# Kernel tuning notes

Measured on AMD Instinct MI355X. Metric: run time of the kernel, lower is better.

The kernel has to match this reference:

```python
import jax, jax.numpy as jnp
import numpy as np

B, L, S, D, H = 2, 384, 384, 512, 256
BASE_TEMP = 10.0
LN_EPS = 1e-5


def setup_inputs() -> dict:
    key = jax.random.key(0)
    ks = jax.random.split(key, 12)
    return {
        "q": jax.random.normal(ks[0], (B, L, D), jnp.float32),
        "k": jax.random.normal(ks[1], (B, S, D), jnp.float32),
        "q_global": jax.random.normal(ks[2], (B, D), jnp.float32),
        "k_global": jax.random.normal(ks[3], (B, D), jnp.float32),
        "W1": jax.random.normal(ks[4], (4 * D, H), jnp.float32) * (1.0 / np.sqrt(4 * D)),
        "b1": jnp.zeros((H,), jnp.float32),
        "gamma": jnp.ones((H,), jnp.float32),
        "beta": jnp.zeros((H,), jnp.float32),
        "W2": jax.random.normal(ks[5], (H, 1), jnp.float32) * (1.0 / np.sqrt(H)),
        "b2": jnp.zeros((1,), jnp.float32),
        "gumbel_u": jax.random.uniform(ks[6], (B, L, S, 2), jnp.float32),
    }


def reference(q, k, q_global, k_global, W1, b1, gamma, beta, W2, b2, gumbel_u):
    d = q.shape[-1]
    # Decompose Linear(4D,H) on the [q, k, q_global, k_global] concat into
    # four per-tensor projections; sum broadcasts to the pairwise grid.
    Wq, Wk, Wqg, Wkg = jnp.split(W1, 4, axis=0)  # each [D,H]
    hq = q @ Wq + (q_global @ Wqg)[:, None, :]   # [B,L,H]
    hk = k @ Wk + (k_global @ Wkg)[:, None, :]   # [B,S,H]
    h = hq[:, :, None, :] + hk[:, None, :, :] + b1  # [B,L,S,H]
    h = jax.nn.gelu(h, approximate=False)
    mu = jnp.mean(h, axis=-1, keepdims=True)
    var = jnp.mean(jnp.square(h - mu), axis=-1, keepdims=True)
    h = (h - mu) * jax.lax.rsqrt(var + LN_EPS) * gamma + beta
    thresholds = (h @ W2)[..., 0] + b2[0]  # [B,L,S]
    sim = jnp.einsum("bld,bsd->bls", q, k) / jnp.sqrt(jnp.float32(d))
    logits = (sim - thresholds) / BASE_TEMP
    binary_logits = jnp.stack([-logits, logits], axis=-1)  # [B,L,S,2]
    u = jnp.clip(gumbel_u, 1e-6, 1.0 - 1e-6)
    g = -jnp.log(-jnp.log(u))
    soft = jax.nn.softmax(binary_logits + g, axis=-1)  # tau=1.0
    hard = jax.nn.one_hot(jnp.argmax(soft, axis=-1), 2, dtype=soft.dtype)
    y = hard + soft - jax.lax.stop_gradient(soft)  # straight-through
    return y[..., 1][:, None, :, :]  # [B,1,L,S]
```

## Files before the change

kernel.cpp:

```cpp
#include <hip/hip_runtime.h>
#include <hip/hip_bf16.h>
#include <math.h>

#define Bb 2
#define Lq 384
#define Sk 384
#define Dd 512
#define Hh 256

#define LIST_CAP 65536
#define NROWS (2 * Bb * Lq)

#define HQD_OFF  0
#define HKD_OFF  (HQD_OFF + Bb*Lq*Hh*8)
#define PART_OFF (HKD_OFF + Bb*Sk*Hh*8)
#define GQD_OFF  (PART_OFF + NROWS*4*Hh*8)
#define GKD_OFF  (GQD_OFF + Bb*Hh*8)
#define HQ_OFF   (GKD_OFF + Bb*Hh*8)
#define HK_OFF   (HQ_OFF + Bb*Lq*Hh*4)
#define SIM0_OFF (HK_OFF + Bb*Sk*Hh*4)
#define SIM1_OFF (SIM0_OFF + Bb*Lq*Sk*4)
#define SCAL_OFF (SIM1_OFF + Bb*Lq*Sk*4)
#define CNT_OFF  (SCAL_OFF + 64)
#define LIST_OFF (CNT_OFF + 64)

__global__ __launch_bounds__(256) void smalls_kernel(
    const float* __restrict__ qg, const float* __restrict__ kg,
    const float* __restrict__ W1,
    const float* __restrict__ gam, const float* __restrict__ bet,
    const float* __restrict__ W2, const float* __restrict__ b2,
    double* __restrict__ gq_d, double* __restrict__ gk_d,
    float* __restrict__ scal, int* __restrict__ cnt)
{
    __shared__ double red[64][5];
    __shared__ float2 red2[256];
    int bx  = blockIdx.x;
    int tid = threadIdx.x;
    if (bx < 16) {
        int isK = bx & 1;
        int b   = (bx >> 1) & 1;
        int hc  = bx >> 2;
        int hl  = tid >> 2;
        int dp  = tid & 3;
        int h   = hc * 64 + hl;
        const float* gv = (isK ? kg : qg) + b * Dd;
        const float* wp = W1 + (isK ? 3 : 2) * Dd * Hh + h;
        int d0 = dp * 128;
        double a0 = 0, a1 = 0, a2 = 0, a3 = 0;
        for (int i = 0; i < 128; i += 4) {
            int d = d0 + i;
            a0 = fma((double)gv[d + 0], (double)wp[(d + 0) * Hh], a0);
            a1 = fma((double)gv[d + 1], (double)wp[(d + 1) * Hh], a1);
            a2 = fma((double)gv[d + 2], (double)wp[(d + 2) * Hh], a2);
            a3 = fma((double)gv[d + 3], (double)wp[(d + 3) * Hh], a3);
        }
        red[hl][dp] = ((a0 + a1) + (a2 + a3));
        __syncthreads();
        if (dp == 0) {
            double s = (red[hl][0] + red[hl][1]) + (red[hl][2] + red[hl][3]);
            (isK ? gk_d : gq_d)[b * Hh + h] = s;
        }
    } else {
        if (tid == 0) *cnt = 0;
        float w2v = W2[tid];
        red2[tid] = make_float2(gam[tid] * w2v, bet[tid] * w2v);
        __syncthreads();
        for (int o = 128; o > 0; o >>= 1) {
            if (tid < o) {
                red2[tid].x += red2[tid + o].x;
                red2[tid].y += red2[tid + o].y;
            }
            __syncthreads();
        }
        if (tid == 0) {
            scal[0] = red2[0].x;
            scal[1] = red2[0].y + b2[0];
        }
    }
}

__global__ __launch_bounds__(256) void projd_part_kernel(
    const float* __restrict__ q, const float* __restrict__ k,
    const float* __restrict__ W1, double* __restrict__ part)
{
    __shared__ __align__(16) float tile[4][128];
    int tid = threadIdx.x;
    int bx  = blockIdx.x;
    int ds  = bx & 3;
    int rgid = bx >> 2;
    bool isQ = rgid < 192;
    int bb = isQ ? rgid : rgid - 192;
    int b  = bb / 96;
    int rg = bb % 96;
    const float* src = isQ ? q : k;
    int woff = isQ ? 0 : Dd * Hh;
    int rowbase = b * Lq + rg * 4;

    if (tid < 128) {
        int row = tid >> 5;
        int c4  = (tid & 31) << 2;
        *reinterpret_cast<float4*>(&tile[row][c4]) =
            *reinterpret_cast<const float4*>(
                src + (size_t)(rowbase + row) * Dd + ds * 128 + c4);
    }
    __syncthreads();

    const float* wp = W1 + woff + (ds * 128) * Hh + tid;
    double a0 = 0.0, a1 = 0.0, a2 = 0.0, a3 = 0.0;
#pragma unroll 2
    for (int d4 = 0; d4 < 128; d4 += 4) {
        double w0 = (double)wp[(d4 + 0) * Hh];
        double w1 = (double)wp[(d4 + 1) * Hh];
        double w2 = (double)wp[(d4 + 2) * Hh];
        double w3 = (double)wp[(d4 + 3) * Hh];
        float4 t0 = *reinterpret_cast<const float4*>(&tile[0][d4]);
        float4 t1 = *reinterpret_cast<const float4*>(&tile[1][d4]);
        float4 t2 = *reinterpret_cast<const float4*>(&tile[2][d4]);
        float4 t3 = *reinterpret_cast<const float4*>(&tile[3][d4]);
        a0 = fma((double)t0.x, w0, a0); a0 = fma((double)t0.y, w1, a0);
        a0 = fma((double)t0.z, w2, a0); a0 = fma((double)t0.w, w3, a0);
        a1 = fma((double)t1.x, w0, a1); a1 = fma((double)t1.y, w1, a1);
        a1 = fma((double)t1.z, w2, a1); a1 = fma((double)t1.w, w3, a1);
        a2 = fma((double)t2.x, w0, a2); a2 = fma((double)t2.y, w1, a2);
        a2 = fma((double)t2.z, w2, a2); a2 = fma((double)t2.w, w3, a2);
        a3 = fma((double)t3.x, w0, a3); a3 = fma((double)t3.y, w1, a3);
        a3 = fma((double)t3.z, w2, a3); a3 = fma((double)t3.w, w3, a3);
    }
    int rowglob = (isQ ? 0 : Bb * Lq) + rowbase;
    size_t obase = ((size_t)rowglob * 4 + ds) * Hh + tid;
    part[obase]            = a0;
    part[obase + 4 * Hh]   = a1;
    part[obase + 8 * Hh]   = a2;
    part[obase + 12 * Hh]  = a3;
}

__global__ __launch_bounds__(256) void finalize_kernel(
    const double* __restrict__ part,
    const double* __restrict__ gq_d, const double* __restrict__ gk_d,
    const float* __restrict__ b1,
    double* __restrict__ hq_d, double* __restrict__ hk_d,
    float* __restrict__ hq, float* __restrict__ hk)
{
    int tid = threadIdx.x;
    int bx  = blockIdx.x;
#pragma unroll
    for (int r = 0; r < 2; ++r) {
        int rowglob = bx * 2 + r;
        bool isQ = rowglob < Bb * Lq;
        int rr = isQ ? rowglob : rowglob - Bb * Lq;
        int b  = rr / Lq;
        size_t pbase = ((size_t)rowglob * 4) * Hh + tid;
        double p0 = part[pbase];
        double p1 = part[pbase + 1 * Hh];
        double p2 = part[pbase + 2 * Hh];
        double p3 = part[pbase + 3 * Hh];
        double gl = (isQ ? gq_d : gk_d)[b * Hh + tid];
        double tot = ((p0 + p1) + (p2 + p3)) + gl;
        size_t o = (size_t)rr * Hh + tid;
        if (isQ) {
            hq_d[o] = tot;
            hq[o]   = (float)(tot + (double)b1[tid]);
        } else {
            hk_d[o] = tot;
            hk[o]   = (float)tot;
        }
    }
}

__global__ __launch_bounds__(256) void sim_kernel(
    const float* __restrict__ q, const float* __restrict__ k,
    float* __restrict__ sim01)
{
    __shared__ __align__(16) float qs[32][132];
    __shared__ __align__(16) float ks[32][132];
    int tid = threadIdx.x;
    int bx = blockIdx.x;
    int kc = (bx >= Bb * 144) ? 1 : 0;
    int r  = bx - kc * Bb * 144;
    int b  = r / 144;  r %= 144;
    int lt = r / 12, st = r % 12;
    int tl = tid >> 4, ts = tid & 15;
    const float* qb = q + (b * Lq + lt * 32) * Dd;
    const float* kb = k + (b * Sk + st * 32) * Dd;
    float a00 = 0.f, a01 = 0.f, a10 = 0.f, a11 = 0.f;
    for (int c = kc * 256; c < kc * 256 + 256; c += 128) {
        __syncthreads();
        for (int i = tid; i < 1024; i += 256) {
            int row = i >> 5;
            int c4  = (i & 31) << 2;
            *reinterpret_cast<float4*>(&qs[row][c4]) =
                *reinterpret_cast<const float4*>(qb + row * Dd + c + c4);
            *reinterpret_cast<float4*>(&ks[row][c4]) =
                *reinterpret_cast<const float4*>(kb + row * Dd + c + c4);
        }
        __syncthreads();
#pragma unroll 2
        for (int dd = 0; dd < 128; dd += 4) {
            float4 q0 = *reinterpret_cast<const float4*>(&qs[tl][dd]);
            float4 q1 = *reinterpret_cast<const float4*>(&qs[tl + 16][dd]);
            float4 k0 = *reinterpret_cast<const float4*>(&ks[ts][dd]);
            float4 k1 = *reinterpret_cast<const float4*>(&ks[ts + 16][dd]);
            a00 = fmaf(q0.x, k0.x, a00); a00 = fmaf(q0.y, k0.y, a00);
            a00 = fmaf(q0.z, k0.z, a00); a00 = fmaf(q0.w, k0.w, a00);
            a01 = fmaf(q0.x, k1.x, a01); a01 = fmaf(q0.y, k1.y, a01);
            a01 = fmaf(q0.z, k1.z, a01); a01 = fmaf(q0.w, k1.w, a01);
            a10 = fmaf(q1.x, k0.x, a10); a10 = fmaf(q1.y, k0.y, a10);
            a10 = fmaf(q1.z, k0.z, a10); a10 = fmaf(q1.w, k0.w, a10);
            a11 = fmaf(q1.x, k1.x, a11); a11 = fmaf(q1.y, k1.y, a11);
            a11 = fmaf(q1.z, k1.z, a11); a11 = fmaf(q1.w, k1.w, a11);
        }
    }
    const float sc = 0.04419417382415922f;
    float* dst = sim01 + kc * (Bb * Lq * Sk);
    int l0 = lt * 32 + tl, s0 = st * 32 + ts;
    dst[(b * Lq + l0)      * Sk + s0]      = a00 * sc;
    dst[(b * Lq + l0)      * Sk + s0 + 16] = a01 * sc;
    dst[(b * Lq + l0 + 16) * Sk + s0]      = a10 * sc;
    dst[(b * Lq + l0 + 16) * Sk + s0 + 16] = a11 * sc;
}

__device__ __forceinline__ void gelu2(float2 hqv, float2 hkv, float2 gwv,
                                      float2& s1, float2& s2, float2& sw)
{
    const float P2   = 0.23164189f;
    const float A1f = 0.254829592f, A2f = -0.284496736f, A3f = 1.421413741f,
                A4f = -1.453152027f, A5f = 1.061405429f;
    const float NL2EH = -0.72134752044448170f;

    float xa = hqv.x + hkv.x,        xb = hqv.y + hkv.y;
    float axa = fabsf(xa),           axb = fabsf(xb);
    float dda = fmaf(P2, axa, 1.0f), ddb = fmaf(P2, axb, 1.0f);
    float ta = __builtin_amdgcn_rcpf(dda), tb = __builtin_amdgcn_rcpf(ddb);
    float x2a = xa * xa,             x2b = xb * xb;
    float exa = __builtin_amdgcn_exp2f(x2a * NL2EH);
    float exb = __builtin_amdgcn_exp2f(x2b * NL2EH);
    float sa = fmaf(A5f, ta, A4f),   sb = fmaf(A5f, tb, A4f);
    sa = fmaf(sa, ta, A3f);          sb = fmaf(sb, tb, A3f);
    sa = fmaf(sa, ta, A2f);          sb = fmaf(sb, tb, A2f);
    sa = fmaf(sa, ta, A1f);          sb = fmaf(sb, tb, A1f);
    sa = sa * ta;                    sb = sb * tb;
    float Ea = fmaf(-sa, exa, 1.0f), Eb = fmaf(-sb, exb, 1.0f);
    float ya = fmaf(axa, Ea, xa),    yb = fmaf(axb, Eb, xb);
    s1.x += ya;                      s1.y += yb;
    s2.x = fmaf(ya, ya, s2.x);       s2.y = fmaf(yb, yb, s2.y);
    sw.x = fmaf(ya, gwv.x, sw.x);    sw.y = fmaf(yb, gwv.y, sw.y);
}

__global__ __launch_bounds__(256) void main_kernel(
    const float* __restrict__ hq, const float* __restrict__ hk,
    const float* __restrict__ sim0, const float* __restrict__ sim1,
    const float* __restrict__ gam, const float* __restrict__ W2,
    const float* __restrict__ scal,
    const float* __restrict__ gu, float* __restrict__ out,
    int* __restrict__ cnt, int* __restrict__ list)
{
    __shared__ __align__(16) float hq_t[32][260];
    __shared__ __align__(16) float hk_t[16][260];
    __shared__ __align__(16) float gw_s[256];
    int tid = threadIdx.x;
    int bx = blockIdx.x;
    int b  = bx / (12 * 24);
    int r  = bx % (12 * 24);
    int lt = r / 24, st = r % 24;

    const float* hqb = hq + (b * Lq + lt * 32) * Hh;
    const float* hkb = hk + (b * Sk + st * 16) * Hh;
#pragma unroll
    for (int i = 0; i < 8; ++i) {
        int idx4 = i * 256 + tid;
        int row  = idx4 >> 6;
        int col4 = (idx4 & 63) << 2;
        *reinterpret_cast<float4*>(&hq_t[row][col4]) =
            *reinterpret_cast<const float4*>(hqb + row * Hh + col4);
    }
#pragma unroll
    for (int i = 0; i < 4; ++i) {
        int idx4 = i * 256 + tid;
        int row  = idx4 >> 6;
        int col4 = (idx4 & 63) << 2;
        *reinterpret_cast<float4*>(&hk_t[row][col4]) =
            *reinterpret_cast<const float4*>(hkb + row * Hh + col4);
    }
    gw_s[tid] = gam[tid] * W2[tid];
    __syncthreads();
    float gwsum  = scal[0];
    float bconst = scal[1];

    int tl = tid >> 4, ts = tid & 15;
    float2 s1a = make_float2(0.f, 0.f), s2a = s1a, swa = s1a;
    float2 s1b = s1a, s2b = s1a, swb = s1a;
#pragma unroll 2
    for (int h4 = 0; h4 < Hh; h4 += 4) {
        float4 ha = *reinterpret_cast<const float4*>(&hq_t[tl][h4]);
        float4 hb = *reinterpret_cast<const float4*>(&hq_t[tl + 16][h4]);
        float4 kk = *reinterpret_cast<const float4*>(&hk_t[ts][h4]);
        float4 g4 = *reinterpret_cast<const float4*>(&gw_s[h4]);
        gelu2(make_float2(ha.x, ha.y), make_float2(kk.x, kk.y),
              make_float2(g4.x, g4.y), s1a, s2a, swa);
        gelu2(make_float2(ha.z, ha.w), make_float2(kk.z, kk.w),
              make_float2(g4.z, g4.w), s1a, s2a, swa);
        gelu2(make_float2(hb.x, hb.y), make_float2(kk.x, kk.y),
              make_float2(g4.x, g4.y), s1b, s2b, swb);
        gelu2(make_float2(hb.z, hb.w), make_float2(kk.z, kk.w),
              make_float2(g4.z, g4.w), s1b, s2b, swb);
    }

#pragma unroll
    for (int e = 0; e < 2; ++e) {
        float S1 = e ? (s1b.x + s1b.y) : (s1a.x + s1a.y);
        float S2 = e ? (s2b.x + s2b.y) : (s2a.x + s2a.y);
        float SW = 0.5f * (e ? (swb.x + swb.y) : (swa.x + swa.y));
        float mu   = S1 * (1.0f / 512.0f);
        float var  = S2 * (1.0f / 1024.0f) - mu * mu;
        float rstd = rsqrtf(var + 1e-5f);
        float thr  = rstd * (SW - mu * gwsum) + bconst;

        int l = lt * 32 + tl + e * 16, s = st * 16 + ts;
        int idx = (b * Lq + l) * Sk + s;
        float  sv = sim0[idx] + sim1[idx];
        float2 uv = reinterpret_cast<const float2*>(gu)[idx];
        float u0 = fminf(fmaxf(uv.x, 1e-6f), 1.0f - 1e-6f);
        float u1 = fminf(fmaxf(uv.y, 1e-6f), 1.0f - 1e-6f);
        float g0 = -logf(-logf(u0));
        float g1 = -logf(-logf(u1));
        float t  = 0.2f * (sv - thr) + (g1 - g0);
        out[idx] = t > 0.0f ? 1.0f : 0.0f;
        if (fabsf(t) < 1e-3f) {
            int p = atomicAdd(cnt, 1);
            if (p < LIST_CAP) list[p] = idx;
        }
    }
}

__global__ __launch_bounds__(256) void cleanup_kernel(
    const float* __restrict__ q, const float* __restrict__ k,
    const double* __restrict__ hq_d, const double* __restrict__ hk_d,
    const float* __restrict__ b1,
    const float* __restrict__ gam, const float* __restrict__ bet,
    const float* __restrict__ W2, const float* __restrict__ b2,
    const float* __restrict__ gu, float* __restrict__ out,
    const int* __restrict__ cnt, const int* __restrict__ list)
{
    __shared__ double s0[256], s1[256], s2[256], s3[256];
    int tid = threadIdx.x;
    int n = *cnt;
    if (n > LIST_CAP) n = LIST_CAP;
    if (n == 0) return;

    double gw  = (double)gam[tid] * (double)W2[tid];
    double b1d = (double)b1[tid];
    s0[tid] = (double)bet[tid] * (double)W2[tid];
    s1[tid] = gw;
    __syncthreads();
    for (int o = 128; o > 0; o >>= 1) {
        if (tid < o) { s0[tid] += s0[tid + o]; s1[tid] += s1[tid + o]; }
        __syncthreads();
    }
    double bconst = s0[0] + (double)b2[0];
    double gwsum  = s1[0];
    __syncthreads();

    for (int it = blockIdx.x; it < n; it += gridDim.x) {
        int idx = list[it];
        int b   = idx / (Lq * Sk);
        int rem = idx % (Lq * Sk);
        int l = rem / Sk, s = rem % Sk;
        double x = (hq_d[(b * Lq + l) * Hh + tid]
                  + hk_d[(b * Sk + s) * Hh + tid]) + b1d;
        double y = 0.5 * x * (1.0 + erf(x * 0.70710678118654752440));
        const float* qrow = q + (b * Lq + l) * Dd;
        const float* krow = k + (b * Sk + s) * Dd;
        double sp = (double)qrow[tid] * (double)krow[tid]
                  + (double)qrow[tid + 256] * (double)krow[tid + 256];
        s0[tid] = y; s1[tid] = y * y; s2[tid] = y * gw; s3[tid] = sp;
        __syncthreads();
        for (int o = 128; o > 0; o >>= 1) {
            if (tid < o) {
                s0[tid] += s0[tid + o]; s1[tid] += s1[tid + o];
                s2[tid] += s2[tid + o]; s3[tid] += s3[tid + o];
            }
            __syncthreads();
        }
        if (tid == 0) {
            double mu   = s0[0] * (1.0 / 256.0);
            double var  = s1[0] * (1.0 / 256.0) - mu * mu;
            double rstd = 1.0 / sqrt(var + 1e-5);
            double thr  = rstd * (s2[0] - mu * gwsum) + bconst;
            double simv = s3[0] / 22.627416997969522;
            float2 uv = reinterpret_cast<const float2*>(gu)[idx];
            double u0 = fmin(fmax((double)uv.x, 1e-6), 1.0 - 1e-6);
            double u1 = fmin(fmax((double)uv.y, 1e-6), 1.0 - 1e-6);
            double g0 = -log(-log(u0));
            double g1 = -log(-log(u1));
            double t  = 0.2 * (simv - thr) + (g1 - g0);
            out[idx] = t > 0.0 ? 1.0f : 0.0f;
        }
        __syncthreads();
    }
}

extern "C" void kernel_launch(void* const* d_in, const int* in_sizes, int n_in,
                              void* d_out, int out_size, void* d_ws, size_t ws_size,
                              hipStream_t stream)
{
    const float* q   = (const float*)d_in[0];
    const float* k   = (const float*)d_in[1];
    const float* qg  = (const float*)d_in[2];
    const float* kg  = (const float*)d_in[3];
    const float* W1  = (const float*)d_in[4];
    const float* b1  = (const float*)d_in[5];
    const float* gam = (const float*)d_in[6];
    const float* bet = (const float*)d_in[7];
    const float* W2  = (const float*)d_in[8];
    const float* b2  = (const float*)d_in[9];
    const float* gu  = (const float*)d_in[10];
    float* out = (float*)d_out;

    char*   ws   = (char*)d_ws;
    double* hq_d = (double*)(ws + HQD_OFF);
    double* hk_d = (double*)(ws + HKD_OFF);
    double* part = (double*)(ws + PART_OFF);
    double* gq_d = (double*)(ws + GQD_OFF);
    double* gk_d = (double*)(ws + GKD_OFF);
    float*  hq   = (float*)(ws + HQ_OFF);
    float*  hk   = (float*)(ws + HK_OFF);
    float*  sim0 = (float*)(ws + SIM0_OFF);
    float*  sim1 = (float*)(ws + SIM1_OFF);
    float*  scal = (float*)(ws + SCAL_OFF);
    int*    cnt  = (int*)(ws + CNT_OFF);
    int*    list = (int*)(ws + LIST_OFF);

    smalls_kernel<<<17, 256, 0, stream>>>(
        qg, kg, W1, gam, bet, W2, b2, gq_d, gk_d, scal, cnt);
    projd_part_kernel<<<NROWS, 256, 0, stream>>>(q, k, W1, part);
    finalize_kernel<<<NROWS / 2, 256, 0, stream>>>(
        part, gq_d, gk_d, b1, hq_d, hk_d, hq, hk);
    sim_kernel<<<2 * Bb * 144, 256, 0, stream>>>(q, k, sim0);
    main_kernel<<<Bb * 12 * 24, 256, 0, stream>>>(
        hq, hk, sim0, sim1, gam, W2, scal, gu, out, cnt, list);
    cleanup_kernel<<<768, 256, 0, stream>>>(
        q, k, hq_d, hk_d, b1, gam, bet, W2, b2, gu, out, cnt, list);
}
```

Before: 171.1 us.

## Use tanh-form GELU, split hidden dim across thread pairs, fuse projection launches

Replaces the erf-polynomial GELU with a cheaper sigmoid/exp2-based approximation, so each element needs one exp2 and one rcp. The main kernel now runs 512 threads per block, with each output pair splitting the H reduction in half and combining partial sums through a lane shuffle. The small global-projection kernel and the per-row projection kernel are merged into one launch. The ambiguous-result band sent to the exact cleanup pass is widened to make up for the looser approximation, which can grow the cleanup list and the atomic traffic.

```diff
diff --git a/kernel.cpp b/kernel.cpp
--- a/kernel.cpp
+++ b/kernel.cpp
@@ -24,16 +24,19 @@
 #define CNT_OFF  (SCAL_OFF + 64)
 #define LIST_OFF (CNT_OFF + 64)
 
-__global__ __launch_bounds__(256) void smalls_kernel(
+__global__ __launch_bounds__(256) void proj_fused_kernel(
+    const float* __restrict__ q, const float* __restrict__ k,
     const float* __restrict__ qg, const float* __restrict__ kg,
     const float* __restrict__ W1,
     const float* __restrict__ gam, const float* __restrict__ bet,
     const float* __restrict__ W2, const float* __restrict__ b2,
     double* __restrict__ gq_d, double* __restrict__ gk_d,
-    float* __restrict__ scal, int* __restrict__ cnt)
+    float* __restrict__ scal, int* __restrict__ cnt,
+    double* __restrict__ part)
 {
     __shared__ double red[64][5];
     __shared__ float2 red2[256];
+    __shared__ __align__(16) float tile[4][128];
     int bx  = blockIdx.x;
     int tid = threadIdx.x;
     if (bx < 16) {
@@ -60,7 +63,7 @@
             double s = (red[hl][0] + red[hl][1]) + (red[hl][2] + red[hl][3]);
             (isK ? gk_d : gq_d)[b * Hh + h] = s;
         }
-    } else {
+    } else if (bx == 16) {
         if (tid == 0) *cnt = 0;
         float w2v = W2[tid];
         red2[tid] = make_float2(gam[tid] * w2v, bet[tid] * w2v);
@@ -76,62 +79,55 @@
             scal[0] = red2[0].x;
             scal[1] = red2[0].y + b2[0];
         }
-    }
-}
-
-__global__ __launch_bounds__(256) void projd_part_kernel(
-    const float* __restrict__ q, const float* __restrict__ k,
-    const float* __restrict__ W1, double* __restrict__ part)
-{
-    __shared__ __align__(16) float tile[4][128];
-    int tid = threadIdx.x;
-    int bx  = blockIdx.x;
-    int ds  = bx & 3;
-    int rgid = bx >> 2;
-    bool isQ = rgid < 192;
-    int bb = isQ ? rgid : rgid - 192;
-    int b  = bb / 96;
-    int rg = bb % 96;
-    const float* src = isQ ? q : k;
-    int woff = isQ ? 0 : Dd * Hh;
-    int rowbase = b * Lq + rg * 4;
-
-    if (tid < 128) {
-        int row = tid >> 5;
-        int c4  = (tid & 31) << 2;
-        *reinterpret_cast<float4*>(&tile[row][c4]) =
-            *reinterpret_cast<const float4*>(
-                src + (size_t)(rowbase + row) * Dd + ds * 128 + c4);
-    }
-    __syncthreads();
-
-    const float* wp = W1 + woff + (ds * 128) * Hh + tid;
-    double a0 = 0.0, a1 = 0.0, a2 = 0.0, a3 = 0.0;
+    } else {
+        int bxp = bx - 17;
+        int ds  = bxp & 3;
+        int rgid = bxp >> 2;
+        bool isQ = rgid < 192;
+        int bb = isQ ? rgid : rgid - 192;
+        int b  = bb / 96;
+        int rg = bb % 96;
+        const float* src = isQ ? q : k;
+        int woff = isQ ? 0 : Dd * Hh;
+        int rowbase = b * Lq + rg * 4;
+
+        if (tid < 128) {
+            int row = tid >> 5;
+            int c4  = (tid & 31) << 2;
+            *reinterpret_cast<float4*>(&tile[row][c4]) =
+                *reinterpret_cast<const float4*>(
+                    src + (size_t)(rowbase + row) * Dd + ds * 128 + c4);
+        }
+        __syncthreads();
+
+        const float* wp = W1 + woff + (ds * 128) * Hh + tid;
+        double a0 = 0.0, a1 = 0.0, a2 = 0.0, a3 = 0.0;
 #pragma unroll 2
-    for (int d4 = 0; d4 < 128; d4 += 4) {
-        double w0 = (double)wp[(d4 + 0) * Hh];
-        double w1 = (double)wp[(d4 + 1) * Hh];
-        double w2 = (double)wp[(d4 + 2) * Hh];
-        double w3 = (double)wp[(d4 + 3) * Hh];
-        float4 t0 = *reinterpret_cast<const float4*>(&tile[0][d4]);
-        float4 t1 = *reinterpret_cast<const float4*>(&tile[1][d4]);
-        float4 t2 = *reinterpret_cast<const float4*>(&tile[2][d4]);
-        float4 t3 = *reinterpret_cast<const float4*>(&tile[3][d4]);
-        a0 = fma((double)t0.x, w0, a0); a0 = fma((double)t0.y, w1, a0);
-        a0 = fma((double)t0.z, w2, a0); a0 = fma((double)t0.w, w3, a0);
-        a1 = fma((double)t1.x, w0, a1); a1 = fma((double)t1.y, w1, a1);
-        a1 = fma((double)t1.z, w2, a1); a1 = fma((double)t1.w, w3, a1);
-        a2 = fma((double)t2.x, w0, a2); a2 = fma((double)t2.y, w1, a2);
-        a2 = fma((double)t2.z, w2, a2); a2 = fma((double)t2.w, w3, a2);
-        a3 = fma((double)t3.x, w0, a3); a3 = fma((double)t3.y, w1, a3);
-        a3 = fma((double)t3.z, w2, a3); a3 = fma((double)t3.w, w3, a3);
-    }
-    int rowglob = (isQ ? 0 : Bb * Lq) + rowbase;
-    size_t obase = ((size_t)rowglob * 4 + ds) * Hh + tid;
-    part[obase]            = a0;
-    part[obase + 4 * Hh]   = a1;
-    part[obase + 8 * Hh]   = a2;
-    part[obase + 12 * Hh]  = a3;
+        for (int d4 = 0; d4 < 128; d4 += 4) {
+            double w0 = (double)wp[(d4 + 0) * Hh];
+            double w1 = (double)wp[(d4 + 1) * Hh];
+            double w2 = (double)wp[(d4 + 2) * Hh];
+            double w3 = (double)wp[(d4 + 3) * Hh];
+            float4 t0 = *reinterpret_cast<const float4*>(&tile[0][d4]);
+            float4 t1 = *reinterpret_cast<const float4*>(&tile[1][d4]);
+            float4 t2 = *reinterpret_cast<const float4*>(&tile[2][d4]);
+            float4 t3 = *reinterpret_cast<const float4*>(&tile[3][d4]);
+            a0 = fma((double)t0.x, w0, a0); a0 = fma((double)t0.y, w1, a0);
+            a0 = fma((double)t0.z, w2, a0); a0 = fma((double)t0.w, w3, a0);
+            a1 = fma((double)t1.x, w0, a1); a1 = fma((double)t1.y, w1, a1);
+            a1 = fma((double)t1.z, w2, a1); a1 = fma((double)t1.w, w3, a1);
+            a2 = fma((double)t2.x, w0, a2); a2 = fma((double)t2.y, w1, a2);
+            a2 = fma((double)t2.z, w2, a2); a2 = fma((double)t2.w, w3, a2);
+            a3 = fma((double)t3.x, w0, a3); a3 = fma((double)t3.y, w1, a3);
+            a3 = fma((double)t3.z, w2, a3); a3 = fma((double)t3.w, w3, a3);
+        }
+        int rowglob = (isQ ? 0 : Bb * Lq) + rowbase;
+        size_t obase = ((size_t)rowglob * 4 + ds) * Hh + tid;
+        part[obase]           = a0;
+        part[obase + 4 * Hh]  = a1;
+        part[obase + 8 * Hh]  = a2;
+        part[obase + 12 * Hh] = a3;
+    }
 }
 
 __global__ __launch_bounds__(256) void finalize_kernel(
@@ -219,34 +215,26 @@
     dst[(b * Lq + l0 + 16) * Sk + s0 + 16] = a11 * sc;
 }
 
-__device__ __forceinline__ void gelu2(float2 hqv, float2 hkv, float2 gwv,
-                                      float2& s1, float2& s2, float2& sw)
-{
-    const float P2   = 0.23164189f;
-    const float A1f = 0.254829592f, A2f = -0.284496736f, A3f = 1.421413741f,
-                A4f = -1.453152027f, A5f = 1.061405429f;
-    const float NL2EH = -0.72134752044448170f;
-
-    float xa = hqv.x + hkv.x,        xb = hqv.y + hkv.y;
-    float axa = fabsf(xa),           axb = fabsf(xb);
-    float dda = fmaf(P2, axa, 1.0f), ddb = fmaf(P2, axb, 1.0f);
-    float ta = __builtin_amdgcn_rcpf(dda), tb = __builtin_amdgcn_rcpf(ddb);
-    float x2a = xa * xa,             x2b = xb * xb;
-    float exa = __builtin_amdgcn_exp2f(x2a * NL2EH);
-    float exb = __builtin_amdgcn_exp2f(x2b * NL2EH);
-    float sa = fmaf(A5f, ta, A4f),   sb = fmaf(A5f, tb, A4f);
-    sa = fmaf(sa, ta, A3f);          sb = fmaf(sb, tb, A3f);
-    sa = fmaf(sa, ta, A2f);          sb = fmaf(sb, tb, A2f);
-    sa = fmaf(sa, ta, A1f);          sb = fmaf(sb, tb, A1f);
-    sa = sa * ta;                    sb = sb * tb;
-    float Ea = fmaf(-sa, exa, 1.0f), Eb = fmaf(-sb, exb, 1.0f);
-    float ya = fmaf(axa, Ea, xa),    yb = fmaf(axb, Eb, xb);
-    s1.x += ya;                      s1.y += yb;
-    s2.x = fmaf(ya, ya, s2.x);       s2.y = fmaf(yb, yb, s2.y);
-    sw.x = fmaf(ya, gwv.x, sw.x);    sw.y = fmaf(yb, gwv.y, sw.y);
-}
-
-__global__ __launch_bounds__(256) void main_kernel(
+__device__ __forceinline__ void gelu2t(float2 hqv, float2 hkv, float2 gwv,
+                                       float2& s1, float2& s2, float2& sw)
+{
+    const float K1 = -2.30220815f;
+    const float K2 = -0.10294325f;
+    float xa = hqv.x + hkv.x,  xb = hqv.y + hkv.y;
+    float x2a = xa * xa,       x2b = xb * xb;
+    float pa = fmaf(K2, x2a, K1), pb = fmaf(K2, x2b, K1);
+    float za = xa * pa,        zb = xb * pb;
+    float ea = __builtin_amdgcn_exp2f(za);
+    float eb = __builtin_amdgcn_exp2f(zb);
+    float ra = __builtin_amdgcn_rcpf(1.0f + ea);
+    float rb = __builtin_amdgcn_rcpf(1.0f + eb);
+    float ya = (xa + xa) * ra, yb = (xb + xb) * rb;
+    s1.x += ya;                s1.y += yb;
+    s2.x = fmaf(ya, ya, s2.x); s2.y = fmaf(yb, yb, s2.y);
+    sw.x = fmaf(ya, gwv.x, sw.x); sw.y = fmaf(yb, gwv.y, sw.y);
+}
+
+__global__ __launch_bounds__(512) void main_kernel(
     const float* __restrict__ hq, const float* __restrict__ hk,
     const float* __restrict__ sim0, const float* __restrict__ sim1,
     const float* __restrict__ gam, const float* __restrict__ W2,
@@ -266,69 +254,76 @@
     const float* hqb = hq + (b * Lq + lt * 32) * Hh;
     const float* hkb = hk + (b * Sk + st * 16) * Hh;
 #pragma unroll
-    for (int i = 0; i < 8; ++i) {
-        int idx4 = i * 256 + tid;
+    for (int i = 0; i < 4; ++i) {
+        int idx4 = i * 512 + tid;
         int row  = idx4 >> 6;
         int col4 = (idx4 & 63) << 2;
         *reinterpret_cast<float4*>(&hq_t[row][col4]) =
             *reinterpret_cast<const float4*>(hqb + row * Hh + col4);
     }
 #pragma unroll
-    for (int i = 0; i < 4; ++i) {
-        int idx4 = i * 256 + tid;
+    for (int i = 0; i < 2; ++i) {
+        int idx4 = i * 512 + tid;
         int row  = idx4 >> 6;
         int col4 = (idx4 & 63) << 2;
         *reinterpret_cast<float4*>(&hk_t[row][col4]) =
             *reinterpret_cast<const float4*>(hkb + row * Hh + col4);
     }
-    gw_s[tid] = gam[tid] * W2[tid];
+    if (tid < 256) gw_s[tid] = gam[tid] * W2[tid];
     __syncthreads();
     float gwsum  = scal[0];
     float bconst = scal[1];
 
-    int tl = tid >> 4, ts = tid & 15;
+    int opair = tid >> 1;
+    int hh    = tid & 1;
+    int tl = opair >> 4, ts = opair & 15;
+
     float2 s1a = make_float2(0.f, 0.f), s2a = s1a, swa = s1a;
     float2 s1b = s1a, s2b = s1a, swb = s1a;
+    int h0 = hh << 7;
 #pragma unroll 2
-    for (int h4 = 0; h4 < Hh; h4 += 4) {
+    for (int h4 = h0; h4 < h0 + 128; h4 += 4) {
         float4 ha = *reinterpret_cast<const float4*>(&hq_t[tl][h4]);
         float4 hb = *reinterpret_cast<const float4*>(&hq_t[tl + 16][h4]);
         float4 kk = *reinterpret_cast<const float4*>(&hk_t[ts][h4]);
         float4 g4 = *reinterpret_cast<const float4*>(&gw_s[h4]);
-        gelu2(make_float2(ha.x, ha.y), make_float2(kk.x, kk.y),
-              make_float2(g4.x, g4.y), s1a, s2a, swa);
-        gelu2(make_float2(ha.z, ha.w), make_float2(kk.z, kk.w),
-              make_float2(g4.z, g4.w), s1a, s2a, swa);
-        gelu2(make_float2(hb.x, hb.y), make_float2(kk.x, kk.y),
-              make_float2(g4.x, g4.y), s1b, s2b, swb);
-        gelu2(make_float2(hb.z, hb.w), make_float2(kk.z, kk.w),
-              make_float2(g4.z, g4.w), s1b, s2b, swb);
-    }
-
-#pragma unroll
-    for (int e = 0; e < 2; ++e) {
-        float S1 = e ? (s1b.x + s1b.y) : (s1a.x + s1a.y);
-        float S2 = e ? (s2b.x + s2b.y) : (s2a.x + s2a.y);
-        float SW = 0.5f * (e ? (swb.x + swb.y) : (swa.x + swa.y));
-        float mu   = S1 * (1.0f / 512.0f);
-        float var  = S2 * (1.0f / 1024.0f) - mu * mu;
-        float rstd = rsqrtf(var + 1e-5f);
-        float thr  = rstd * (SW - mu * gwsum) + bconst;
-
-        int l = lt * 32 + tl + e * 16, s = st * 16 + ts;
-        int idx = (b * Lq + l) * Sk + s;
-        float  sv = sim0[idx] + sim1[idx];
-        float2 uv = reinterpret_cast<const float2*>(gu)[idx];
-        float u0 = fminf(fmaxf(uv.x, 1e-6f), 1.0f - 1e-6f);
-        float u1 = fminf(fmaxf(uv.y, 1e-6f), 1.0f - 1e-6f);
-        float g0 = -logf(-logf(u0));
-        float g1 = -logf(-logf(u1));
-        float t  = 0.2f * (sv - thr) + (g1 - g0);
-        out[idx] = t > 0.0f ? 1.0f : 0.0f;
-        if (fabsf(t) < 1e-3f) {
-            int p = atomicAdd(cnt, 1);
-            if (p < LIST_CAP) list[p] = idx;
-        }
+        gelu2t(make_float2(ha.x, ha.y), make_float2(kk.x, kk.y),
+               make_float2(g4.x, g4.y), s1a, s2a, swa);
+        gelu2t(make_float2(ha.z, ha.w), make_float2(kk.z, kk.w),
+               make_float2(g4.z, g4.w), s1a, s2a, swa);
+        gelu2t(make_float2(hb.x, hb.y), make_float2(kk.x, kk.y),
+               make_float2(g4.x, g4.y), s1b, s2b, swb);
+        gelu2t(make_float2(hb.z, hb.w), make_float2(kk.z, kk.w),
+               make_float2(g4.z, g4.w), s1b, s2b, swb);
+    }
+    float S1a = s1a.x + s1a.y;  S1a += __shfl_xor(S1a, 1, 64);
+    float S2a = s2a.x + s2a.y;  S2a += __shfl_xor(S2a, 1, 64);
+    float SWa = swa.x + swa.y;  SWa += __shfl_xor(SWa, 1, 64);
+    float S1b = s1b.x + s1b.y;  S1b += __shfl_xor(S1b, 1, 64);
+    float S2b = s2b.x + s2b.y;  S2b += __shfl_xor(S2b, 1, 64);
+    float SWb = swb.x + swb.y;  SWb += __shfl_xor(SWb, 1, 64);
+
+    float S1 = hh ? S1b : S1a;
+    float S2 = hh ? S2b : S2a;
+    float SW = 0.5f * (hh ? SWb : SWa);
+    float mu   = S1 * (1.0f / 512.0f);
+    float var  = S2 * (1.0f / 1024.0f) - mu * mu;
+    float rstd = rsqrtf(var + 1e-5f);
+    float thr  = rstd * (SW - mu * gwsum) + bconst;
+
+    int l = lt * 32 + tl + hh * 16, s = st * 16 + ts;
+    int idx = (b * Lq + l) * Sk + s;
+    float  sv = sim0[idx] + sim1[idx];
+    float2 uv = reinterpret_cast<const float2*>(gu)[idx];
+    float u0 = fminf(fmaxf(uv.x, 1e-6f), 1.0f - 1e-6f);
+    float u1 = fminf(fmaxf(uv.y, 1e-6f), 1.0f - 1e-6f);
+    float g0 = -logf(-logf(u0));
+    float g1 = -logf(-logf(u1));
+    float t  = 0.2f * (sv - thr) + (g1 - g0);
+    out[idx] = t > 0.0f ? 1.0f : 0.0f;
+    if (fabsf(t) < 2e-3f) {
+        int p = atomicAdd(cnt, 1);
+        if (p < LIST_CAP) list[p] = idx;
     }
 }
 
@@ -430,13 +425,12 @@
     int*    cnt  = (int*)(ws + CNT_OFF);
     int*    list = (int*)(ws + LIST_OFF);
 
-    smalls_kernel<<<17, 256, 0, stream>>>(
-        qg, kg, W1, gam, bet, W2, b2, gq_d, gk_d, scal, cnt);
-    projd_part_kernel<<<NROWS, 256, 0, stream>>>(q, k, W1, part);
+    proj_fused_kernel<<<17 + NROWS, 256, 0, stream>>>(
+        q, k, qg, kg, W1, gam, bet, W2, b2, gq_d, gk_d, scal, cnt, part);
     finalize_kernel<<<NROWS / 2, 256, 0, stream>>>(
         part, gq_d, gk_d, b1, hq_d, hk_d, hq, hk);
     sim_kernel<<<2 * Bb * 144, 256, 0, stream>>>(q, k, sim0);
-    main_kernel<<<Bb * 12 * 24, 256, 0, stream>>>(
+    main_kernel<<<Bb * 12 * 24, 512, 0, stream>>>(
         hq, hk, sim0, sim1, gam, W2, scal, gu, out, cnt, list);
     cleanup_kernel<<<768, 256, 0, stream>>>(
         q, k, hq_d, hk_d, b1, gam, bet, W2, b2, gu, out, cnt, list);
```

Result: faster. 157.2 us (-8.1%).
